# Optimization experiments

Hardware: AMD Instinct MI355X
Metric: run time of the kernel (lower is better)

Reference implementation:

```python
import jax, jax.numpy as jnp
import numpy as np

T, B, NA = 32, 32, 5          # timesteps, envs, actions
HID, FEAT = 256, 512          # lstm hidden, cnn features
IN_DIM = FEAT + NA            # lstm input size (517)
FLAT = 64 * 7 * 7             # cnn flatten size (3136)


def _conv(x, w, b, s):
    # x: NCHW, w: OIHW, VALID padding, stride s
    y = jax.lax.conv_general_dilated(x, w, (s, s), 'VALID',
                                     dimension_numbers=('NCHW', 'OIHW', 'NCHW'))
    return y + b[None, :, None, None]


def setup_inputs() -> dict:
    key = jax.random.key(0)
    ks = jax.random.split(key, 24)
    p = lambda k, shape: (jax.random.normal(k, shape, jnp.float32) * 0.05)
    return {
        'image': jax.random.uniform(ks[0], (T * B, 3, 84, 84), jnp.float32) * 255.0,
        'last_action': jax.random.randint(ks[1], (T * B,), 0, NA),
        'done': jax.random.bernoulli(ks[2], 0.05, (T * B,)).astype(jnp.float32),
        'h0': jnp.zeros((B, HID), jnp.float32),
        'c0': jnp.zeros((B, HID), jnp.float32),
        # NatureCNN params
        'W1': p(ks[3], (32, 3, 8, 8)), 'b1': jnp.zeros((32,), jnp.float32),
        'W2': p(ks[4], (64, 32, 4, 4)), 'b2': jnp.zeros((64,), jnp.float32),
        'W3': p(ks[5], (64, 64, 3, 3)), 'b3': jnp.zeros((64,), jnp.float32),
        'Wfc': p(ks[6], (FEAT, FLAT)), 'bfc': jnp.zeros((FEAT,), jnp.float32),
        # LSTM params (torch gate order i,f,g,o)
        'W_ih': p(ks[7], (4 * HID, IN_DIM)), 'W_hh': p(ks[8], (4 * HID, HID)),
        'b_ih': jnp.zeros((4 * HID,), jnp.float32), 'b_hh': jnp.zeros((4 * HID,), jnp.float32),
        # policy MLP (hidden 64, tanh)
        'Wp1': p(ks[9], (64, HID)), 'bp1': jnp.zeros((64,), jnp.float32),
        'Wp2': p(ks[10], (NA, 64)) * 0.01, 'bp2': jnp.zeros((NA,), jnp.float32),
        # value MLP
        'Wv1': p(ks[11], (64, HID)), 'bv1': jnp.zeros((64,), jnp.float32),
        'Wv2': p(ks[12], (1, 64)), 'bv2': jnp.zeros((1,), jnp.float32),
    }


def reference(image, last_action, done, h0, c0,
              W1, b1, W2, b2, W3, b3, Wfc, bfc,
              W_ih, W_hh, b_ih, b_hh,
              Wp1, bp1, Wp2, bp2, Wv1, bv1, Wv2, bv2):
    # --- extract: NatureCNN + one-hot(last_action) ---
    x = image / 255.0
    x = jax.nn.relu(_conv(x, W1, b1, 4))   # (TB,32,20,20)
    x = jax.nn.relu(_conv(x, W2, b2, 2))   # (TB,64,9,9)
    x = jax.nn.relu(_conv(x, W3, b3, 1))   # (TB,64,7,7)
    x = x.reshape(x.shape[0], -1)
    feat = jax.nn.relu(x @ Wfc.T + bfc)    # (TB,512)
    oh = jax.nn.one_hot(last_action, NA, dtype=feat.dtype)
    xs = jnp.concatenate([feat, oh], axis=1).reshape(T, B, IN_DIM)
    ds = done.reshape(T, B)

    # --- remember: done-masked LSTM recurrence (torch gate order i,f,g,o) ---
    def step(carry, inp):
        h, c = carry
        xt, dt = inp
        m = (1.0 - dt)[:, None]
        h = h * m
        c = c * m
        g = xt @ W_ih.T + b_ih + h @ W_hh.T + b_hh   # (B, 4*HID)
        i, f, gg, o = jnp.split(g, 4, axis=1)
        c = jax.nn.sigmoid(f) * c + jax.nn.sigmoid(i) * jnp.tanh(gg)
        h = jax.nn.sigmoid(o) * jnp.tanh(c)
        return (h, c), h

    (hT, cT), hs = jax.lax.scan(step, (h0, c0), (xs, ds))
    h = hs.reshape(T * B, HID)

    # --- heads ---
    logits = jnp.tanh(h @ Wp1.T + bp1) @ Wp2.T + bp2   # (TB, NA)
    v = jnp.tanh(h @ Wv1.T + bv1) @ Wv2.T + bv2        # (TB, 1)
    return logits, v, hT, cT
```

## Files before the change

### kernel.cpp

```cpp
#include <hip/hip_runtime.h>
#include <math.h>

typedef float  f4v __attribute__((ext_vector_type(4)));
typedef short  s8v __attribute__((ext_vector_type(8)));
typedef int    i4v __attribute__((ext_vector_type(4)));

__device__ __forceinline__ float sigm(float x) { return 1.f / (1.f + expf(-x)); }
__device__ __forceinline__ unsigned short f2bf(float f) {
    unsigned int u = __float_as_uint(f);
    return (unsigned short)((u + 0x7FFF + ((u >> 16) & 1)) >> 16);
}
__device__ __forceinline__ unsigned int cvt2(float lo, float hi) {
    unsigned int r;
    asm("v_cvt_pk_bf16_f32 %0, %1, %2" : "=v"(r) : "v"(lo), "v"(hi));
    return r;
}
__device__ __forceinline__ s8v pack8(float4 a, float4 b) {
    union { unsigned int u[4]; s8v v; } r;
    r.u[0] = cvt2(a.x, a.y); r.u[1] = cvt2(a.z, a.w);
    r.u[2] = cvt2(b.x, b.y); r.u[3] = cvt2(b.z, b.w);
    return r.v;
}

__global__ __launch_bounds__(256) void k_amax(const float* __restrict__ Whh,
                                              unsigned int* __restrict__ amax_bits) {
    int i = blockIdx.x * 256 + threadIdx.x;
    float v = fabsf(Whh[i]);
#pragma unroll
    for (int o = 1; o < 64; o <<= 1) v = fmaxf(v, __shfl_xor(v, o));
    if ((threadIdx.x & 63) == 0) atomicMax(amax_bits, __float_as_uint(v));
}

__global__ __launch_bounds__(256) void k_prep(const float* __restrict__ W2, const float* __restrict__ W3,
                                              const float* __restrict__ Wfc, const float* __restrict__ Wih,
                                              const float* __restrict__ W1, const float* __restrict__ Whh,
                                              const unsigned int* __restrict__ amax_bits,
                                              unsigned short* __restrict__ W2p, unsigned short* __restrict__ W3p,
                                              unsigned short* __restrict__ Wfcp, unsigned short* __restrict__ Wihp,
                                              unsigned short* __restrict__ W1p, signed char* __restrict__ Wq) {
    int i = blockIdx.x * 256 + threadIdx.x;
    if (i < 32768) {
        W2p[i] = f2bf(W2[i]);
    } else if (i < 98304) {
        int j = i - 32768;
        int co = j >> 10, r = j & 1023, ci = r >> 4, s = r & 15, ky = s >> 2, kx = s & 3;
        W3p[j] = (ky < 3 && kx < 3) ? f2bf(W3[((co * 64 + ci) * 3 + ky) * 3 + kx]) : (unsigned short)0;
    } else if (i < 1703936) {
        int j = i - 98304;
        Wfcp[j] = f2bf(Wfc[j]);
    } else if (i < 2228224) {
        int j = i - 1703936;
        int n = j >> 9, k = j & 511;
        Wihp[j] = f2bf(Wih[n * 517 + k]);
    } else if (i < 2234368) {
        int j = i - 2228224;
        W1p[j] = f2bf(W1[j] * (1.f / 255.f));
    } else if (i < 2496512) {
        int j = i - 2234368;
        float amax = __uint_as_float(amax_bits[0]);
        float s = 127.f / amax;
        int qv = (int)rintf(Whh[j] * s);
        qv = qv > 127 ? 127 : (qv < -127 ? -127 : qv);
        Wq[j] = (signed char)qv;
    }
}

__global__ __launch_bounds__(256) void k_conv1(const float* __restrict__ img,
                                               const unsigned short* __restrict__ Bw,
                                               const float* __restrict__ bias,
                                               unsigned short* __restrict__ out) {
    __shared__ unsigned short c1s[32][132];
    int lane = threadIdx.x & 63, w = threadIdx.x >> 6;
    int l15 = lane & 15, q = lane >> 4;
    int m0 = blockIdx.x * 128;
    const float* Ap[2];
#pragma unroll
    for (int mf = 0; mf < 2; ++mf) {
        int m = m0 + w * 32 + mf * 16 + l15;
        int im = m / 400, p = m - im * 400;
        int oy = p / 20, ox = p - oy * 20;
        Ap[mf] = img + im * 21168 + oy * 336 + ox * 4;
    }
    const unsigned short* Bp0 = Bw + l15 * 192 + q * 8;
    const unsigned short* Bp1 = Bw + (16 + l15) * 192 + q * 8;
    s8v bf0[6], bf1[6];
#pragma unroll
    for (int ks = 0; ks < 6; ++ks) {
        bf0[ks] = *(const s8v*)(Bp0 + ks * 32);
        bf1[ks] = *(const s8v*)(Bp1 + ks * 32);
    }
    int roffs[6];
#pragma unroll
    for (int ks = 0; ks < 6; ++ks) {
        int k0 = ks * 32 + q * 8;
        int c = k0 >> 6, ky = (k0 >> 3) & 7;
        roffs[ks] = c * 7056 + ky * 84;
    }
    f4v acc[4];
#pragma unroll
    for (int i = 0; i < 4; ++i) acc[i] = (f4v){0.f, 0.f, 0.f, 0.f};
    float4 ca[2], cb[2];
#pragma unroll
    for (int mf = 0; mf < 2; ++mf) {
        ca[mf] = *(const float4*)(Ap[mf] + roffs[0]);
        cb[mf] = *(const float4*)(Ap[mf] + roffs[0] + 4);
    }
#pragma unroll
    for (int ks = 0; ks < 6; ++ks) {
        float4 na[2], nb[2];
        if (ks < 5) {
#pragma unroll
            for (int mf = 0; mf < 2; ++mf) {
                na[mf] = *(const float4*)(Ap[mf] + roffs[ks + 1]);
                nb[mf] = *(const float4*)(Ap[mf] + roffs[ks + 1] + 4);
            }
        }
#pragma unroll
        for (int mf = 0; mf < 2; ++mf) {
            s8v ua = pack8(ca[mf], cb[mf]);
            acc[mf * 2 + 0] = __builtin_amdgcn_mfma_f32_16x16x32_bf16(ua, bf0[ks], acc[mf * 2 + 0], 0, 0, 0);
            acc[mf * 2 + 1] = __builtin_amdgcn_mfma_f32_16x16x32_bf16(ua, bf1[ks], acc[mf * 2 + 1], 0, 0, 0);
        }
        if (ks < 5) {
#pragma unroll
            for (int mf = 0; mf < 2; ++mf) { ca[mf] = na[mf]; cb[mf] = nb[mf]; }
        }
    }
#pragma unroll
    for (int nf = 0; nf < 2; ++nf) {
        int n = nf * 16 + l15;
        float b = bias[n];
#pragma unroll
        for (int mf = 0; mf < 2; ++mf) {
            int ml = w * 32 + mf * 16 + q * 4;
#pragma unroll
            for (int r = 0; r < 4; r += 2) {
                float v0 = acc[mf * 2 + nf][r] + b;     v0 = v0 > 0.f ? v0 : 0.f;
                float v1 = acc[mf * 2 + nf][r + 1] + b; v1 = v1 > 0.f ? v1 : 0.f;
                *(unsigned int*)&c1s[n][ml + r] = cvt2(v0, v1);
            }
        }
    }
    __syncthreads();
#pragma unroll
    for (int seg = 0; seg < 16; ++seg) {
        int flat = seg * 256 + threadIdx.x;
        int n = flat >> 7, ml = flat & 127;
        int m = m0 + ml;
        int im = m / 400, p = m - im * 400;
        out[(im * 32 + n) * 400 + p] = c1s[n][ml];
    }
}

__global__ __launch_bounds__(256) void k_conv2(const unsigned short* __restrict__ A,
                                               const unsigned short* __restrict__ Bw,
                                               const float* __restrict__ bias,
                                               unsigned short* __restrict__ out) {
    __shared__ unsigned short c2s[32][136];
    int lane = threadIdx.x & 63, w = threadIdx.x >> 6;
    int l15 = lane & 15, q = lane >> 4;
    int m0 = blockIdx.x * 128;
    int n0 = blockIdx.y * 32;
    int ma = m0 + w * 32 + l15, mb = ma + 16;
    int ia = ma / 81, pa = ma - ia * 81; int oya = pa / 9, oxa = pa - oya * 9;
    int ib = mb / 81, pb = mb - ib * 81; int oyb = pb / 9, oxb = pb - oyb * 9;
    const unsigned short* Aa = A + ia * 12800 + oya * 40 + oxa * 2 + (q & 1) * 40;
    const unsigned short* Ab = A + ib * 12800 + oyb * 40 + oxb * 2 + (q & 1) * 40;
    int ci0 = q >> 1;
    const unsigned short* B0 = Bw + (n0 + l15) * 512 + q * 8;
    const unsigned short* B1 = B0 + 16 * 512;
    f4v acc[4];
#pragma unroll
    for (int i = 0; i < 4; ++i) acc[i] = (f4v){0.f, 0.f, 0.f, 0.f};
    union AU { unsigned int u[4]; s8v v; };
    const unsigned short* pa_ = Aa + ci0 * 400;
    const unsigned short* pb_ = Ab + ci0 * 400;
    AU ua, ub;
    ua.u[0] = *(const unsigned int*)(pa_);      ua.u[1] = *(const unsigned int*)(pa_ + 2);
    ua.u[2] = *(const unsigned int*)(pa_ + 20); ua.u[3] = *(const unsigned int*)(pa_ + 22);
    ub.u[0] = *(const unsigned int*)(pb_);      ub.u[1] = *(const unsigned int*)(pb_ + 2);
    ub.u[2] = *(const unsigned int*)(pb_ + 20); ub.u[3] = *(const unsigned int*)(pb_ + 22);
    s8v b0 = *(const s8v*)B0, b1 = *(const s8v*)B1;
    for (int c = 0; c < 16; ++c) {
        AU nua, nub; s8v nb0, nb1;
        if (c < 15) {
            pa_ += 800; pb_ += 800; B0 += 32; B1 += 32;
            nua.u[0] = *(const unsigned int*)(pa_);      nua.u[1] = *(const unsigned int*)(pa_ + 2);
            nua.u[2] = *(const unsigned int*)(pa_ + 20); nua.u[3] = *(const unsigned int*)(pa_ + 22);
            nub.u[0] = *(const unsigned int*)(pb_);      nub.u[1] = *(const unsigned int*)(pb_ + 2);
            nub.u[2] = *(const unsigned int*)(pb_ + 20); nub.u[3] = *(const unsigned int*)(pb_ + 22);
            nb0 = *(const s8v*)B0; nb1 = *(const s8v*)B1;
        }
        acc[0] = __builtin_amdgcn_mfma_f32_16x16x32_bf16(ua.v, b0, acc[0], 0, 0, 0);
        acc[1] = __builtin_amdgcn_mfma_f32_16x16x32_bf16(ua.v, b1, acc[1], 0, 0, 0);
        acc[2] = __builtin_amdgcn_mfma_f32_16x16x32_bf16(ub.v, b0, acc[2], 0, 0, 0);
        acc[3] = __builtin_amdgcn_mfma_f32_16x16x32_bf16(ub.v, b1, acc[3], 0, 0, 0);
        if (c < 15) { ua = nua; ub = nub; b0 = nb0; b1 = nb1; }
    }
#pragma unroll
    for (int nf = 0; nf < 2; ++nf) {
        int nl = nf * 16 + l15;
        float b = bias[n0 + nl];
#pragma unroll
        for (int mf = 0; mf < 2; ++mf) {
            int ml = w * 32 + mf * 16 + q * 4;
#pragma unroll
            for (int r = 0; r < 4; r += 2) {
                float v0 = acc[mf * 2 + nf][r] + b;     v0 = v0 > 0.f ? v0 : 0.f;
                float v1 = acc[mf * 2 + nf][r + 1] + b; v1 = v1 > 0.f ? v1 : 0.f;
                *(unsigned int*)&c2s[nl][ml + r] = cvt2(v0, v1);
            }
        }
    }
    __syncthreads();
#pragma unroll
    for (int seg = 0; seg < 16; ++seg) {
        int flat = seg * 256 + threadIdx.x;
        int nl = flat >> 7, ml = flat & 127;
        int n = n0 + nl;
        int m = m0 + ml;
        int im = m / 81, p = m - im * 81;
        out[im * 5184 + n * 81 + p] = c2s[nl][ml];
    }
}

__global__ __launch_bounds__(256) void k_conv3(const unsigned short* __restrict__ A,
                                               const unsigned short* __restrict__ Bw,
                                               const float* __restrict__ bias,
                                               unsigned short* __restrict__ out) {
    __shared__ unsigned short c3s[32][68];
    int lane = threadIdx.x & 63, w = threadIdx.x >> 6;
    int l15 = lane & 15, q = lane >> 4;
    int m0 = blockIdx.x * 64;
    int n0 = blockIdx.y * 32;
    int ma = m0 + w * 16 + l15;
    int ia = ma / 49, pa = ma - ia * 49; int oya = pa / 7, oxa = pa - oya * 7;
    int ky0 = (q & 1) * 2;
    int r0off = ky0 * 9;
    int r1off = (ky0 + 1 > 2 ? 2 : ky0 + 1) * 9;
    int zr = q & 1;
    const unsigned short* Aa = A + ia * 5184 + oya * 9 + oxa;
    int ci0 = q >> 1;
    const unsigned short* B0 = Bw + (n0 + l15) * 1024 + q * 8;
    const unsigned short* B1 = B0 + 16 * 1024;
    f4v acc[2];
    acc[0] = (f4v){0.f, 0.f, 0.f, 0.f};
    acc[1] = (f4v){0.f, 0.f, 0.f, 0.f};
    const unsigned short* pa_ = Aa + ci0 * 81;
    unsigned short ca_[6];
    ca_[0] = pa_[r0off]; ca_[1] = pa_[r0off + 1]; ca_[2] = pa_[r0off + 2];
    ca_[3] = pa_[r1off]; ca_[4] = pa_[r1off + 1]; ca_[5] = pa_[r1off + 2];
    s8v b0 = *(const s8v*)B0, b1 = *(const s8v*)B1;
    for (int c = 0; c < 32; ++c) {
        unsigned short na_[6]; s8v nb0, nb1;
        if (c < 31) {
            pa_ += 162; B0 += 32; B1 += 32;
            na_[0] = pa_[r0off]; na_[1] = pa_[r0off + 1]; na_[2] = pa_[r0off + 2];
            na_[3] = pa_[r1off]; na_[4] = pa_[r1off + 1]; na_[5] = pa_[r1off + 2];
            nb0 = *(const s8v*)B0; nb1 = *(const s8v*)B1;
        }
        s8v av;
        av[0] = (short)ca_[0]; av[1] = (short)ca_[1]; av[2] = (short)ca_[2]; av[3] = 0;
        av[4] = zr ? (short)0 : (short)ca_[3];
        av[5] = zr ? (short)0 : (short)ca_[4];
        av[6] = zr ? (short)0 : (short)ca_[5];
        av[7] = 0;
        acc[0] = __builtin_amdgcn_mfma_f32_16x16x32_bf16(av, b0, acc[0], 0, 0, 0);
        acc[1] = __builtin_amdgcn_mfma_f32_16x16x32_bf16(av, b1, acc[1], 0, 0, 0);
        if (c < 31) {
#pragma unroll
            for (int j = 0; j < 6; ++j) ca_[j] = na_[j];
            b0 = nb0; b1 = nb1;
        }
    }
#pragma unroll
    for (int nf = 0; nf < 2; ++nf) {
        int nl = nf * 16 + l15;
        float b = bias[n0 + nl];
        int ml = w * 16 + q * 4;
#pragma unroll
        for (int r = 0; r < 4; r += 2) {
            float v0 = acc[nf][r] + b;     v0 = v0 > 0.f ? v0 : 0.f;
            float v1 = acc[nf][r + 1] + b; v1 = v1 > 0.f ? v1 : 0.f;
            *(unsigned int*)&c3s[nl][ml + r] = cvt2(v0, v1);
        }
    }
    __syncthreads();
#pragma unroll
    for (int seg = 0; seg < 8; ++seg) {
        int flat = seg * 256 + threadIdx.x;
        int nl = flat >> 6, ml = flat & 63;
        int n = n0 + nl;
        int m = m0 + ml;
        int im = m / 49, p = m - im * 49;
        out[im * 3136 + n * 49 + p] = c3s[nl][ml];
    }
}

__global__ __launch_bounds__(256) void k_fc(const unsigned short* __restrict__ A,
                                            const unsigned short* __restrict__ Bw,
                                            const float* __restrict__ bias,
                                            unsigned short* __restrict__ out) {
    int lane = threadIdx.x & 63, w = threadIdx.x >> 6;
    int l15 = lane & 15, q = lane >> 4;
    int m0 = blockIdx.x * 32 + (w & 1) * 16;
    int n0 = blockIdx.y * 64 + (w >> 1) * 32;
    const unsigned short* Ap = A + (m0 + l15) * 3136 + q * 8;
    const unsigned short* B0 = Bw + (n0 + l15) * 3136 + q * 8;
    const unsigned short* B1 = B0 + 16 * 3136;
    f4v acc0 = (f4v){0.f, 0.f, 0.f, 0.f}, acc1 = (f4v){0.f, 0.f, 0.f, 0.f};
    s8v av = *(const s8v*)Ap, b0 = *(const s8v*)B0, b1 = *(const s8v*)B1;
    for (int c = 0; c < 97; ++c) {
        Ap += 32; B0 += 32; B1 += 32;
        s8v nav = *(const s8v*)Ap, nb0 = *(const s8v*)B0, nb1 = *(const s8v*)B1;
        acc0 = __builtin_amdgcn_mfma_f32_16x16x32_bf16(av, b0, acc0, 0, 0, 0);
        acc1 = __builtin_amdgcn_mfma_f32_16x16x32_bf16(av, b1, acc1, 0, 0, 0);
        av = nav; b0 = nb0; b1 = nb1;
    }
    acc0 = __builtin_amdgcn_mfma_f32_16x16x32_bf16(av, b0, acc0, 0, 0, 0);
    acc1 = __builtin_amdgcn_mfma_f32_16x16x32_bf16(av, b1, acc1, 0, 0, 0);
    float bi0 = bias[n0 + l15], bi1 = bias[n0 + 16 + l15];
#pragma unroll
    for (int r = 0; r < 4; ++r) {
        int m = m0 + q * 4 + r;
        float v0 = acc0[r] + bi0; v0 = v0 > 0.f ? v0 : 0.f;
        float v1 = acc1[r] + bi1; v1 = v1 > 0.f ? v1 : 0.f;
        out[m * 512 + n0 + l15] = f2bf(v0);
        out[m * 512 + n0 + 16 + l15] = f2bf(v1);
    }
}

__global__ __launch_bounds__(256) void k_gx(const unsigned short* __restrict__ A,
                                            const unsigned short* __restrict__ Bw,
                                            const float* __restrict__ Wih,
                                            const float* __restrict__ bih,
                                            const float* __restrict__ bhh,
                                            const int* __restrict__ act,
                                            float* __restrict__ out) {
    int lane = threadIdx.x & 63, w = threadIdx.x >> 6;
    int l15 = lane & 15, q = lane >> 4;
    int m0 = blockIdx.x * 32 + (w & 1) * 16;
    int n0 = blockIdx.y * 64 + (w >> 1) * 32;
    const unsigned short* Ap = A + (m0 + l15) * 512 + q * 8;
    const unsigned short* B0 = Bw + (n0 + l15) * 512 + q * 8;
    const unsigned short* B1 = B0 + 16 * 512;
    f4v acc0 = (f4v){0.f, 0.f, 0.f, 0.f}, acc1 = (f4v){0.f, 0.f, 0.f, 0.f};
    for (int c = 0; c < 16; ++c) {
        s8v av = *(const s8v*)Ap;
        s8v b0 = *(const s8v*)B0;
        s8v b1 = *(const s8v*)B1;
        Ap += 32; B0 += 32; B1 += 32;
        acc0 = __builtin_amdgcn_mfma_f32_16x16x32_bf16(av, b0, acc0, 0, 0, 0);
        acc1 = __builtin_amdgcn_mfma_f32_16x16x32_bf16(av, b1, acc1, 0, 0, 0);
    }
    int na = n0 + l15, nb = n0 + 16 + l15;
    float ca = bih[na] + bhh[na], cb_ = bih[nb] + bhh[nb];
#pragma unroll
    for (int r = 0; r < 4; ++r) {
        int m = m0 + q * 4 + r;
        int a = act[m];
        out[m * 1024 + na] = acc0[r] + Wih[na * 517 + 512 + a] + ca;
        out[m * 1024 + nb] = acc1[r] + Wih[nb * 517 + 512 + a] + cb_;
    }
}

__global__ __launch_bounds__(1024) void k_lstm_all(const float* __restrict__ h0,
                                                   const float* __restrict__ c0,
                                                   const float* __restrict__ done,
                                                   const float* __restrict__ gx,
                                                   const signed char* __restrict__ Wq,
                                                   const unsigned int* __restrict__ amax_bits,
                                                   float* __restrict__ hs,
                                                   float* __restrict__ cb) {
    int b = blockIdx.x;
    int tid = threadIdx.x;
    int w = tid >> 6, lane = tid & 63;
    int l15 = lane & 15, q = lane >> 4;
    __shared__ float gbuf[1024];
    __shared__ float cst[256];
    __shared__ signed char hA[4][64][16];

    i4v wfr[4][4];
    const signed char* wb = Wq + (w * 64 + l15) * 256 + q * 16;
#pragma unroll
    for (int s = 0; s < 4; ++s)
#pragma unroll
        for (int kf = 0; kf < 4; ++kf)
            wfr[s][kf] = *(const i4v*)(wb + s * 16 * 256 + kf * 64);
    float sw = __uint_as_float(amax_bits[0]) * (1.f / (127.f * 127.f));

    ((int*)hA)[tid] = 0;
    __syncthreads();
    if (tid < 256) {
        int u = tid;
        cst[u] = c0[b * 256 + u];
        float m0v = 1.f - done[b];
        float hv = h0[b * 256 + u] * m0v;
        hv = hv > 1.f ? 1.f : (hv < -1.f ? -1.f : hv);
        hA[u >> 6][((u >> 4) & 3) * 16][u & 15] = (signed char)(int)rintf(hv * 127.f);
    }
    __syncthreads();

    for (int t = 0; t < 32; ++t) {
        float gxi = 0.f, gxf = 0.f, gxg = 0.f, gxo = 0.f, dcur = 0.f, dnxt = 0.f;
        if (tid < 256) {
            const float* gr = gx + (t * 32 + b) * 1024;
            gxi = gr[tid]; gxf = gr[256 + tid]; gxg = gr[512 + tid]; gxo = gr[768 + tid];
            dcur = done[t * 32 + b];
            dnxt = (t < 31) ? done[(t + 1) * 32 + b] : 1.f;
        }
        i4v acc[4];
#pragma unroll
        for (int s = 0; s < 4; ++s) acc[s] = (i4v){0, 0, 0, 0};
#pragma unroll
        for (int kf = 0; kf < 4; ++kf) {
            i4v a = *(const i4v*)&hA[kf][lane][0];
#pragma unroll
            for (int s = 0; s < 4; ++s)
                acc[s] = __builtin_amdgcn_mfma_i32_16x16x64_i8(a, wfr[s][kf], acc[s], 0, 0, 0);
        }
        if (q == 0) {
#pragma unroll
            for (int s = 0; s < 4; ++s)
                gbuf[w * 64 + s * 16 + l15] = (float)acc[s][0];
        }
        __syncthreads();
        if (tid < 256) {
            int u = tid;
            float gi = gbuf[u] * sw + gxi;
            float gf = gbuf[256 + u] * sw + gxf;
            float gg = gbuf[512 + u] * sw + gxg;
            float go = gbuf[768 + u] * sw + gxo;
            float cm = cst[u] * (1.f - dcur);
            float cn = sigm(gf) * cm + sigm(gi) * tanhf(gg);
            float hn = sigm(go) * tanhf(cn);
            cst[u] = cn;
            hs[t * 8192 + b * 256 + u] = hn;
            float hv = hn * (1.f - dnxt);
            hA[u >> 6][((u >> 4) & 3) * 16][u & 15] = (signed char)(int)rintf(hv * 127.f);
        }
        __syncthreads();
    }
    if (tid < 256) cb[b * 256 + tid] = cst[tid];
}

__global__ __launch_bounds__(256) void k_heads(const float* __restrict__ hs,
                                               const float* __restrict__ cb,
                                               const float* __restrict__ Wp1, const float* __restrict__ bp1,
                                               const float* __restrict__ Wp2, const float* __restrict__ bp2,
                                               const float* __restrict__ Wv1, const float* __restrict__ bv1,
                                               const float* __restrict__ Wv2, const float* __restrict__ bv2,
                                               float* __restrict__ out) {
    int lane = threadIdx.x & 63;
    int m = blockIdx.x * 4 + (threadIdx.x >> 6);
    const float4* hv = (const float4*)(hs + m * 256);
    const float4* wp = (const float4*)(Wp1 + lane * 256);
    const float4* wq = (const float4*)(Wv1 + lane * 256);
    float ap = 0.f, av = 0.f;
#pragma unroll 8
    for (int k = 0; k < 64; ++k) {
        float4 h4 = hv[k];
        float4 p4 = wp[k];
        float4 q4 = wq[k];
        ap += h4.x * p4.x + h4.y * p4.y + h4.z * p4.z + h4.w * p4.w;
        av += h4.x * q4.x + h4.y * q4.y + h4.z * q4.z + h4.w * q4.w;
    }
    float hp = tanhf(ap + bp1[lane]);
    float hq = tanhf(av + bv1[lane]);
#pragma unroll
    for (int j = 0; j < 5; ++j) {
        float s = hp * Wp2[j * 64 + lane];
        s += __shfl_xor(s, 1); s += __shfl_xor(s, 2); s += __shfl_xor(s, 4);
        s += __shfl_xor(s, 8); s += __shfl_xor(s, 16); s += __shfl_xor(s, 32);
        if (lane == 0) out[m * 5 + j] = s + bp2[j];
    }
    float s = hq * Wv2[lane];
    s += __shfl_xor(s, 1); s += __shfl_xor(s, 2); s += __shfl_xor(s, 4);
    s += __shfl_xor(s, 8); s += __shfl_xor(s, 16); s += __shfl_xor(s, 32);
    if (lane == 0) out[5120 + m] = s + bv2[0];

    int g = blockIdx.x * 256 + threadIdx.x;
    if (g < 8192) {
        out[6144 + g] = hs[31 * 8192 + g];
        out[6144 + 8192 + g] = cb[g];
    }
}

extern "C" void kernel_launch(void* const* d_in, const int* in_sizes, int n_in,
                              void* d_out, int out_size, void* d_ws, size_t ws_size,
                              hipStream_t stream) {
    const float* image = (const float*)d_in[0];
    const int*   act   = (const int*)d_in[1];
    const float* done  = (const float*)d_in[2];
    const float* h0    = (const float*)d_in[3];
    const float* c0    = (const float*)d_in[4];
    const float* W1    = (const float*)d_in[5];
    const float* b1    = (const float*)d_in[6];
    const float* W2    = (const float*)d_in[7];
    const float* b2    = (const float*)d_in[8];
    const float* W3    = (const float*)d_in[9];
    const float* b3    = (const float*)d_in[10];
    const float* Wfc   = (const float*)d_in[11];
    const float* bfc   = (const float*)d_in[12];
    const float* Wih   = (const float*)d_in[13];
    const float* Whh   = (const float*)d_in[14];
    const float* bih   = (const float*)d_in[15];
    const float* bhh   = (const float*)d_in[16];
    const float* Wp1   = (const float*)d_in[17];
    const float* bp1   = (const float*)d_in[18];
    const float* Wp2   = (const float*)d_in[19];
    const float* bp2   = (const float*)d_in[20];
    const float* Wv1   = (const float*)d_in[21];
    const float* bv1   = (const float*)d_in[22];
    const float* Wv2   = (const float*)d_in[23];
    const float* bv2   = (const float*)d_in[24];
    float* out = (float*)d_out;
    char* base = (char*)d_ws;

    unsigned short* a1   = (unsigned short*)(base);
    unsigned short* a2   = (unsigned short*)(base + 26214432);
    unsigned short* W2p  = (unsigned short*)(base + 36831328);
    unsigned short* W3p  = W2p + 32768;
    unsigned short* Wfcp = W2p + 98304;
    unsigned short* Wihp = W2p + 1703936;
    unsigned short* W1p  = (unsigned short*)(base + 41287776);
    unsigned int*   amax = (unsigned int*)(base + 41300064);
    signed char*    Wq   = (signed char*)(base + 41300096);
    unsigned short* a3   = (unsigned short*)(base);
    unsigned short* feat = (unsigned short*)(base + 6422528);
    float* gx = (float*)(base + 7471104);
    float* hs = (float*)(base + 11665408);
    float* cb = (float*)(base + 12713984);

    hipMemsetAsync(amax, 0, 4, stream);
    k_amax<<<1024, 256, 0, stream>>>(Whh, amax);
    k_prep<<<9752, 256, 0, stream>>>(W2, W3, Wfc, Wih, W1, Whh, amax, W2p, W3p, Wfcp, Wihp, W1p, Wq);
    k_conv1<<<3200, 256, 0, stream>>>(image, W1p, b1, a1);
    k_conv2<<<dim3(648, 2), 256, 0, stream>>>(a1, W2p, b2, a2);
    k_conv3<<<dim3(784, 2), 256, 0, stream>>>(a2, W3p, b3, a3);
    k_fc<<<dim3(32, 8), 256, 0, stream>>>(a3, Wfcp, bfc, feat);
    k_gx<<<dim3(32, 16), 256, 0, stream>>>(feat, Wihp, Wih, bih, bhh, act, gx);
    k_lstm_all<<<32, 1024, 0, stream>>>(h0, c0, done, gx, Wq, amax, hs, cb);
    k_heads<<<256, 256, 0, stream>>>(hs, cb, Wp1, bp1, Wp2, bp2, Wv1, bv1, Wv2, bv2, out);
}
```

Baseline: 485.6 us.

## Stage conv2/conv3 input images in swizzled LDS and compute all channels per block

conv2 and conv3 now load two whole images' activations into LDS with an XOR swizzle and a channel-innermost layout. Each block then computes all 64 output channels with implicit-GEMM MFMAs over kernel taps, instead of gathering scattered 2-byte global loads per K-chunk across two channel-half blocks. Weights are repacked in prep into tap-major, channel-inner order, and conv3's zero padding of its 3x3 taps to 16 is removed. conv1's explicit software prefetch is dropped in favour of direct loads. The risks are higher LDS use per block, limiting occupancy, and redundant MFMA work on padded rows in partial tiles.

```diff
diff --git a/kernel.cpp b/kernel.cpp
--- a/kernel.cpp
+++ b/kernel.cpp
@@ -40,23 +40,25 @@
                                               unsigned short* __restrict__ W1p, signed char* __restrict__ Wq) {
     int i = blockIdx.x * 256 + threadIdx.x;
     if (i < 32768) {
-        W2p[i] = f2bf(W2[i]);
-    } else if (i < 98304) {
+        int co = i >> 9, k = i & 511, t = k >> 5, ci = k & 31, ky = t >> 2, kx = t & 3;
+        W2p[i] = f2bf(W2[co * 512 + ci * 16 + ky * 4 + kx]);
+    } else if (i < 69632) {
         int j = i - 32768;
-        int co = j >> 10, r = j & 1023, ci = r >> 4, s = r & 15, ky = s >> 2, kx = s & 3;
-        W3p[j] = (ky < 3 && kx < 3) ? f2bf(W3[((co * 64 + ci) * 3 + ky) * 3 + kx]) : (unsigned short)0;
-    } else if (i < 1703936) {
-        int j = i - 98304;
+        int co = j / 576, k = j - co * 576, t = k >> 6, ci = k & 63;
+        int ky = t / 3, kx = t - ky * 3;
+        W3p[j] = f2bf(W3[((co * 64 + ci) * 3 + ky) * 3 + kx]);
+    } else if (i < 1675264) {
+        int j = i - 69632;
         Wfcp[j] = f2bf(Wfc[j]);
-    } else if (i < 2228224) {
-        int j = i - 1703936;
+    } else if (i < 2199552) {
+        int j = i - 1675264;
         int n = j >> 9, k = j & 511;
         Wihp[j] = f2bf(Wih[n * 517 + k]);
-    } else if (i < 2234368) {
-        int j = i - 2228224;
+    } else if (i < 2205696) {
+        int j = i - 2199552;
         W1p[j] = f2bf(W1[j] * (1.f / 255.f));
-    } else if (i < 2496512) {
-        int j = i - 2234368;
+    } else if (i < 2467840) {
+        int j = i - 2205696;
         float amax = __uint_as_float(amax_bits[0]);
         float s = 127.f / amax;
         int qv = (int)rintf(Whh[j] * s);
@@ -99,31 +101,15 @@
     f4v acc[4];
 #pragma unroll
     for (int i = 0; i < 4; ++i) acc[i] = (f4v){0.f, 0.f, 0.f, 0.f};
-    float4 ca[2], cb[2];
-#pragma unroll
-    for (int mf = 0; mf < 2; ++mf) {
-        ca[mf] = *(const float4*)(Ap[mf] + roffs[0]);
-        cb[mf] = *(const float4*)(Ap[mf] + roffs[0] + 4);
-    }
 #pragma unroll
     for (int ks = 0; ks < 6; ++ks) {
-        float4 na[2], nb[2];
-        if (ks < 5) {
-#pragma unroll
-            for (int mf = 0; mf < 2; ++mf) {
-                na[mf] = *(const float4*)(Ap[mf] + roffs[ks + 1]);
-                nb[mf] = *(const float4*)(Ap[mf] + roffs[ks + 1] + 4);
-            }
-        }
 #pragma unroll
         for (int mf = 0; mf < 2; ++mf) {
-            s8v ua = pack8(ca[mf], cb[mf]);
+            float4 a0 = *(const float4*)(Ap[mf] + roffs[ks]);
+            float4 a1 = *(const float4*)(Ap[mf] + roffs[ks] + 4);
+            s8v ua = pack8(a0, a1);
             acc[mf * 2 + 0] = __builtin_amdgcn_mfma_f32_16x16x32_bf16(ua, bf0[ks], acc[mf * 2 + 0], 0, 0, 0);
             acc[mf * 2 + 1] = __builtin_amdgcn_mfma_f32_16x16x32_bf16(ua, bf1[ks], acc[mf * 2 + 1], 0, 0, 0);
-        }
-        if (ks < 5) {
-#pragma unroll
-            for (int mf = 0; mf < 2; ++mf) { ca[mf] = na[mf]; cb[mf] = nb[mf]; }
         }
     }
 #pragma unroll
@@ -152,148 +138,188 @@
     }
 }
 
-__global__ __launch_bounds__(256) void k_conv2(const unsigned short* __restrict__ A,
-                                               const unsigned short* __restrict__ Bw,
-                                               const float* __restrict__ bias,
-                                               unsigned short* __restrict__ out) {
-    __shared__ unsigned short c2s[32][136];
-    int lane = threadIdx.x & 63, w = threadIdx.x >> 6;
+__global__ __launch_bounds__(256, 2) void k_conv2(const unsigned short* __restrict__ A,
+                                                  const unsigned short* __restrict__ Bw,
+                                                  const float* __restrict__ bias,
+                                                  unsigned short* __restrict__ out) {
+    __shared__ unsigned short sA[800 * 32];
+    __shared__ unsigned short c2s[64][196];
+    int tid = threadIdx.x;
+    int lane = tid & 63, w = tid >> 6;
     int l15 = lane & 15, q = lane >> 4;
-    int m0 = blockIdx.x * 128;
-    int n0 = blockIdx.y * 32;
-    int ma = m0 + w * 32 + l15, mb = ma + 16;
-    int ia = ma / 81, pa = ma - ia * 81; int oya = pa / 9, oxa = pa - oya * 9;
-    int ib = mb / 81, pb = mb - ib * 81; int oyb = pb / 9, oxb = pb - oyb * 9;
-    const unsigned short* Aa = A + ia * 12800 + oya * 40 + oxa * 2 + (q & 1) * 40;
-    const unsigned short* Ab = A + ib * 12800 + oyb * 40 + oxb * 2 + (q & 1) * 40;
-    int ci0 = q >> 1;
-    const unsigned short* B0 = Bw + (n0 + l15) * 512 + q * 8;
-    const unsigned short* B1 = B0 + 16 * 512;
-    f4v acc[4];
-#pragma unroll
-    for (int i = 0; i < 4; ++i) acc[i] = (f4v){0.f, 0.f, 0.f, 0.f};
-    union AU { unsigned int u[4]; s8v v; };
-    const unsigned short* pa_ = Aa + ci0 * 400;
-    const unsigned short* pb_ = Ab + ci0 * 400;
-    AU ua, ub;
-    ua.u[0] = *(const unsigned int*)(pa_);      ua.u[1] = *(const unsigned int*)(pa_ + 2);
-    ua.u[2] = *(const unsigned int*)(pa_ + 20); ua.u[3] = *(const unsigned int*)(pa_ + 22);
-    ub.u[0] = *(const unsigned int*)(pb_);      ub.u[1] = *(const unsigned int*)(pb_ + 2);
-    ub.u[2] = *(const unsigned int*)(pb_ + 20); ub.u[3] = *(const unsigned int*)(pb_ + 22);
-    s8v b0 = *(const s8v*)B0, b1 = *(const s8v*)B1;
-    for (int c = 0; c < 16; ++c) {
-        AU nua, nub; s8v nb0, nb1;
-        if (c < 15) {
-            pa_ += 800; pb_ += 800; B0 += 32; B1 += 32;
-            nua.u[0] = *(const unsigned int*)(pa_);      nua.u[1] = *(const unsigned int*)(pa_ + 2);
-            nua.u[2] = *(const unsigned int*)(pa_ + 20); nua.u[3] = *(const unsigned int*)(pa_ + 22);
-            nub.u[0] = *(const unsigned int*)(pb_);      nub.u[1] = *(const unsigned int*)(pb_ + 2);
-            nub.u[2] = *(const unsigned int*)(pb_ + 20); nub.u[3] = *(const unsigned int*)(pb_ + 22);
-            nb0 = *(const s8v*)B0; nb1 = *(const s8v*)B1;
-        }
-        acc[0] = __builtin_amdgcn_mfma_f32_16x16x32_bf16(ua.v, b0, acc[0], 0, 0, 0);
-        acc[1] = __builtin_amdgcn_mfma_f32_16x16x32_bf16(ua.v, b1, acc[1], 0, 0, 0);
-        acc[2] = __builtin_amdgcn_mfma_f32_16x16x32_bf16(ub.v, b0, acc[2], 0, 0, 0);
-        acc[3] = __builtin_amdgcn_mfma_f32_16x16x32_bf16(ub.v, b1, acc[3], 0, 0, 0);
-        if (c < 15) { ua = nua; ub = nub; b0 = nb0; b1 = nb1; }
-    }
-#pragma unroll
-    for (int nf = 0; nf < 2; ++nf) {
-        int nl = nf * 16 + l15;
-        float b = bias[n0 + nl];
+    int img0 = blockIdx.x * 2;
+    char* sAb = (char*)sA;
+    const s8v* srcv = (const s8v*)(A + img0 * 12800);
+    for (int wi = tid; wi < 3200; wi += 256) {
+        s8v v = srcv[wi];
+        int f = wi * 8;
+        int im = f / 12800, r = f - im * 12800, ci = r / 400, p = r - ci * 400;
+#pragma unroll
+        for (int j = 0; j < 8; ++j) {
+            int R = im * 400 + p + j;
+            int Rl = (R >> 1) + (R & 1) * 400;
+            int by = (Rl * 32 + ci) * 2 ^ ((Rl & 7) << 4);
+            *(unsigned short*)(sAb + by) = (unsigned short)v[j];
+        }
+    }
+    __syncthreads();
+    int Rb[3];
+#pragma unroll
+    for (int mf = 0; mf < 3; ++mf) {
+        int t = w * 3 + mf;
+        int im = t / 6;
+        int pp = (t - im * 6) * 16 + l15;
+        int px = pp > 80 ? 80 : pp;
+        int oy = px / 9, ox = px - oy * 9;
+        Rb[mf] = im * 400 + oy * 40 + ox * 2;
+    }
+    const unsigned short* Bp0 = Bw + l15 * 512 + q * 8;
+    const unsigned short* Bp1 = Bw + (16 + l15) * 512 + q * 8;
+    const unsigned short* Bp2 = Bw + (32 + l15) * 512 + q * 8;
+    const unsigned short* Bp3 = Bw + (48 + l15) * 512 + q * 8;
+    f4v acc[3][4];
+#pragma unroll
+    for (int i = 0; i < 3; ++i)
+#pragma unroll
+        for (int j = 0; j < 4; ++j) acc[i][j] = (f4v){0.f, 0.f, 0.f, 0.f};
+#pragma unroll
+    for (int s = 0; s < 16; ++s) {
+        const int ky = s >> 2, kx = s & 3;
+        const int d = ky * 20 + kx;
+        s8v a[3];
+#pragma unroll
+        for (int mf = 0; mf < 3; ++mf) {
+            int R = Rb[mf] + d;
+            int Rl = (R >> 1) + (R & 1) * 400;
+            int by = (Rl * 64 + q * 16) ^ ((Rl & 7) << 4);
+            a[mf] = *(const s8v*)(sAb + by);
+        }
+        s8v b0 = *(const s8v*)(Bp0 + s * 32);
+        s8v b1 = *(const s8v*)(Bp1 + s * 32);
+        s8v b2 = *(const s8v*)(Bp2 + s * 32);
+        s8v b3 = *(const s8v*)(Bp3 + s * 32);
+#pragma unroll
+        for (int mf = 0; mf < 3; ++mf) {
+            acc[mf][0] = __builtin_amdgcn_mfma_f32_16x16x32_bf16(a[mf], b0, acc[mf][0], 0, 0, 0);
+            acc[mf][1] = __builtin_amdgcn_mfma_f32_16x16x32_bf16(a[mf], b1, acc[mf][1], 0, 0, 0);
+            acc[mf][2] = __builtin_amdgcn_mfma_f32_16x16x32_bf16(a[mf], b2, acc[mf][2], 0, 0, 0);
+            acc[mf][3] = __builtin_amdgcn_mfma_f32_16x16x32_bf16(a[mf], b3, acc[mf][3], 0, 0, 0);
+        }
+    }
+#pragma unroll
+    for (int nf = 0; nf < 4; ++nf) {
+        int co = nf * 16 + l15;
+        float b = bias[co];
+#pragma unroll
+        for (int mf = 0; mf < 3; ++mf) {
+            int rr = (w * 3 + mf) * 16 + q * 4;
+#pragma unroll
+            for (int r = 0; r < 4; r += 2) {
+                float v0 = acc[mf][nf][r] + b;     v0 = v0 > 0.f ? v0 : 0.f;
+                float v1 = acc[mf][nf][r + 1] + b; v1 = v1 > 0.f ? v1 : 0.f;
+                *(unsigned int*)&c2s[co][rr + r] = cvt2(v0, v1);
+            }
+        }
+    }
+    __syncthreads();
+    for (int idx = tid; idx < 10368; idx += 256) {
+        int im = idx / 5184, r2 = idx - im * 5184, co = r2 / 81, p = r2 - co * 81;
+        out[(img0 + im) * 5184 + r2] = c2s[co][im * 96 + p];
+    }
+}
+
+__global__ __launch_bounds__(256, 2) void k_conv3(const unsigned short* __restrict__ A,
+                                                  const unsigned short* __restrict__ Bw,
+                                                  const float* __restrict__ bias,
+                                                  unsigned short* __restrict__ out) {
+    __shared__ unsigned short sA[162 * 64];
+    __shared__ unsigned short c3s[64][132];
+    int tid = threadIdx.x;
+    int lane = tid & 63, w = tid >> 6;
+    int l15 = lane & 15, q = lane >> 4;
+    int img0 = blockIdx.x * 2;
+    char* sAb = (char*)sA;
+    const s8v* srcv = (const s8v*)(A + img0 * 5184);
+    for (int wi = tid; wi < 1296; wi += 256) {
+        s8v v = srcv[wi];
+        int f = wi * 8;
+#pragma unroll
+        for (int j = 0; j < 8; ++j) {
+            int fe = f + j;
+            int im = fe / 5184, r = fe - im * 5184, ci = r / 81, p = r - ci * 81;
+            int R = im * 81 + p;
+            int by = (R * 64 + ci) * 2 ^ ((R & 7) << 4);
+            *(unsigned short*)(sAb + by) = (unsigned short)v[j];
+        }
+    }
+    __syncthreads();
+    int Rb[2];
+#pragma unroll
+    for (int mf = 0; mf < 2; ++mf) {
+        int t = w * 2 + mf;
+        int im = t >> 2;
+        int pp = (t & 3) * 16 + l15;
+        int px = pp > 48 ? 48 : pp;
+        int oy = px / 7, ox = px - oy * 7;
+        Rb[mf] = im * 81 + oy * 9 + ox;
+    }
+    const unsigned short* Bp0 = Bw + l15 * 576 + q * 8;
+    const unsigned short* Bp1 = Bw + (16 + l15) * 576 + q * 8;
+    const unsigned short* Bp2 = Bw + (32 + l15) * 576 + q * 8;
+    const unsigned short* Bp3 = Bw + (48 + l15) * 576 + q * 8;
+    f4v acc[2][4];
+#pragma unroll
+    for (int i = 0; i < 2; ++i)
+#pragma unroll
+        for (int j = 0; j < 4; ++j) acc[i][j] = (f4v){0.f, 0.f, 0.f, 0.f};
+#pragma unroll
+    for (int s = 0; s < 18; ++s) {
+        const int tap = s >> 1, cb2 = (s & 1) * 64;
+        const int ky = tap / 3, kx = tap - ky * 3;
+        const int d = ky * 9 + kx;
+        s8v a0, a1;
+        {
+            int R = Rb[0] + d;
+            int by = (R * 128 + cb2 + q * 16) ^ ((R & 7) << 4);
+            a0 = *(const s8v*)(sAb + by);
+        }
+        {
+            int R = Rb[1] + d;
+            int by = (R * 128 + cb2 + q * 16) ^ ((R & 7) << 4);
+            a1 = *(const s8v*)(sAb + by);
+        }
+        s8v b0 = *(const s8v*)(Bp0 + s * 32);
+        s8v b1 = *(const s8v*)(Bp1 + s * 32);
+        s8v b2 = *(const s8v*)(Bp2 + s * 32);
+        s8v b3 = *(const s8v*)(Bp3 + s * 32);
+        acc[0][0] = __builtin_amdgcn_mfma_f32_16x16x32_bf16(a0, b0, acc[0][0], 0, 0, 0);
+        acc[0][1] = __builtin_amdgcn_mfma_f32_16x16x32_bf16(a0, b1, acc[0][1], 0, 0, 0);
+        acc[0][2] = __builtin_amdgcn_mfma_f32_16x16x32_bf16(a0, b2, acc[0][2], 0, 0, 0);
+        acc[0][3] = __builtin_amdgcn_mfma_f32_16x16x32_bf16(a0, b3, acc[0][3], 0, 0, 0);
+        acc[1][0] = __builtin_amdgcn_mfma_f32_16x16x32_bf16(a1, b0, acc[1][0], 0, 0, 0);
+        acc[1][1] = __builtin_amdgcn_mfma_f32_16x16x32_bf16(a1, b1, acc[1][1], 0, 0, 0);
+        acc[1][2] = __builtin_amdgcn_mfma_f32_16x16x32_bf16(a1, b2, acc[1][2], 0, 0, 0);
+        acc[1][3] = __builtin_amdgcn_mfma_f32_16x16x32_bf16(a1, b3, acc[1][3], 0, 0, 0);
+    }
+#pragma unroll
+    for (int nf = 0; nf < 4; ++nf) {
+        int co = nf * 16 + l15;
+        float b = bias[co];
 #pragma unroll
         for (int mf = 0; mf < 2; ++mf) {
-            int ml = w * 32 + mf * 16 + q * 4;
+            int rr = (w * 2 + mf) * 16 + q * 4;
 #pragma unroll
             for (int r = 0; r < 4; r += 2) {
-                float v0 = acc[mf * 2 + nf][r] + b;     v0 = v0 > 0.f ? v0 : 0.f;
-                float v1 = acc[mf * 2 + nf][r + 1] + b; v1 = v1 > 0.f ? v1 : 0.f;
-                *(unsigned int*)&c2s[nl][ml + r] = cvt2(v0, v1);
+                float v0 = acc[mf][nf][r] + b;     v0 = v0 > 0.f ? v0 : 0.f;
+                float v1 = acc[mf][nf][r + 1] + b; v1 = v1 > 0.f ? v1 : 0.f;
+                *(unsigned int*)&c3s[co][rr + r] = cvt2(v0, v1);
             }
         }
     }
     __syncthreads();
-#pragma unroll
-    for (int seg = 0; seg < 16; ++seg) {
-        int flat = seg * 256 + threadIdx.x;
-        int nl = flat >> 7, ml = flat & 127;
-        int n = n0 + nl;
-        int m = m0 + ml;
-        int im = m / 81, p = m - im * 81;
-        out[im * 5184 + n * 81 + p] = c2s[nl][ml];
-    }
-}
-
-__global__ __launch_bounds__(256) void k_conv3(const unsigned short* __restrict__ A,
-                                               const unsigned short* __restrict__ Bw,
-                                               const float* __restrict__ bias,
-                                               unsigned short* __restrict__ out) {
-    __shared__ unsigned short c3s[32][68];
-    int lane = threadIdx.x & 63, w = threadIdx.x >> 6;
-    int l15 = lane & 15, q = lane >> 4;
-    int m0 = blockIdx.x * 64;
-    int n0 = blockIdx.y * 32;
-    int ma = m0 + w * 16 + l15;
-    int ia = ma / 49, pa = ma - ia * 49; int oya = pa / 7, oxa = pa - oya * 7;
-    int ky0 = (q & 1) * 2;
-    int r0off = ky0 * 9;
-    int r1off = (ky0 + 1 > 2 ? 2 : ky0 + 1) * 9;
-    int zr = q & 1;
-    const unsigned short* Aa = A + ia * 5184 + oya * 9 + oxa;
-    int ci0 = q >> 1;
-    const unsigned short* B0 = Bw + (n0 + l15) * 1024 + q * 8;
-    const unsigned short* B1 = B0 + 16 * 1024;
-    f4v acc[2];
-    acc[0] = (f4v){0.f, 0.f, 0.f, 0.f};
-    acc[1] = (f4v){0.f, 0.f, 0.f, 0.f};
-    const unsigned short* pa_ = Aa + ci0 * 81;
-    unsigned short ca_[6];
-    ca_[0] = pa_[r0off]; ca_[1] = pa_[r0off + 1]; ca_[2] = pa_[r0off + 2];
-    ca_[3] = pa_[r1off]; ca_[4] = pa_[r1off + 1]; ca_[5] = pa_[r1off + 2];
-    s8v b0 = *(const s8v*)B0, b1 = *(const s8v*)B1;
-    for (int c = 0; c < 32; ++c) {
-        unsigned short na_[6]; s8v nb0, nb1;
-        if (c < 31) {
-            pa_ += 162; B0 += 32; B1 += 32;
-            na_[0] = pa_[r0off]; na_[1] = pa_[r0off + 1]; na_[2] = pa_[r0off + 2];
-            na_[3] = pa_[r1off]; na_[4] = pa_[r1off + 1]; na_[5] = pa_[r1off + 2];
-            nb0 = *(const s8v*)B0; nb1 = *(const s8v*)B1;
-        }
-        s8v av;
-        av[0] = (short)ca_[0]; av[1] = (short)ca_[1]; av[2] = (short)ca_[2]; av[3] = 0;
-        av[4] = zr ? (short)0 : (short)ca_[3];
-        av[5] = zr ? (short)0 : (short)ca_[4];
-        av[6] = zr ? (short)0 : (short)ca_[5];
-        av[7] = 0;
-        acc[0] = __builtin_amdgcn_mfma_f32_16x16x32_bf16(av, b0, acc[0], 0, 0, 0);
-        acc[1] = __builtin_amdgcn_mfma_f32_16x16x32_bf16(av, b1, acc[1], 0, 0, 0);
-        if (c < 31) {
-#pragma unroll
-            for (int j = 0; j < 6; ++j) ca_[j] = na_[j];
-            b0 = nb0; b1 = nb1;
-        }
-    }
-#pragma unroll
-    for (int nf = 0; nf < 2; ++nf) {
-        int nl = nf * 16 + l15;
-        float b = bias[n0 + nl];
-        int ml = w * 16 + q * 4;
-#pragma unroll
-        for (int r = 0; r < 4; r += 2) {
-            float v0 = acc[nf][r] + b;     v0 = v0 > 0.f ? v0 : 0.f;
-            float v1 = acc[nf][r + 1] + b; v1 = v1 > 0.f ? v1 : 0.f;
-            *(unsigned int*)&c3s[nl][ml + r] = cvt2(v0, v1);
-        }
-    }
-    __syncthreads();
-#pragma unroll
-    for (int seg = 0; seg < 8; ++seg) {
-        int flat = seg * 256 + threadIdx.x;
-        int nl = flat >> 6, ml = flat & 63;
-        int n = n0 + nl;
-        int m = m0 + ml;
-        int im = m / 49, p = m - im * 49;
-        out[im * 3136 + n * 49 + p] = c3s[nl][ml];
+    for (int idx = tid; idx < 6272; idx += 256) {
+        int im = idx / 3136, r2 = idx - im * 3136, co = r2 / 49, p = r2 - co * 49;
+        out[(img0 + im) * 3136 + r2] = c3s[co][im * 64 + p];
     }
 }
 
@@ -520,12 +546,12 @@
     unsigned short* a1   = (unsigned short*)(base);
     unsigned short* a2   = (unsigned short*)(base + 26214432);
     unsigned short* W2p  = (unsigned short*)(base + 36831328);
-    unsigned short* W3p  = W2p + 32768;
-    unsigned short* Wfcp = W2p + 98304;
-    unsigned short* Wihp = W2p + 1703936;
-    unsigned short* W1p  = (unsigned short*)(base + 41287776);
-    unsigned int*   amax = (unsigned int*)(base + 41300064);
-    signed char*    Wq   = (signed char*)(base + 41300096);
+    unsigned short* W3p  = (unsigned short*)(base + 36896864);
+    unsigned short* Wfcp = (unsigned short*)(base + 36970592);
+    unsigned short* Wihp = (unsigned short*)(base + 40181856);
+    unsigned short* W1p  = (unsigned short*)(base + 41230432);
+    unsigned int*   amax = (unsigned int*)(base + 41242752);
+    signed char*    Wq   = (signed char*)(base + 41242784);
     unsigned short* a3   = (unsigned short*)(base);
     unsigned short* feat = (unsigned short*)(base + 6422528);
     float* gx = (float*)(base + 7471104);
@@ -534,10 +560,10 @@
 
     hipMemsetAsync(amax, 0, 4, stream);
     k_amax<<<1024, 256, 0, stream>>>(Whh, amax);
-    k_prep<<<9752, 256, 0, stream>>>(W2, W3, Wfc, Wih, W1, Whh, amax, W2p, W3p, Wfcp, Wihp, W1p, Wq);
+    k_prep<<<9640, 256, 0, stream>>>(W2, W3, Wfc, Wih, W1, Whh, amax, W2p, W3p, Wfcp, Wihp, W1p, Wq);
     k_conv1<<<3200, 256, 0, stream>>>(image, W1p, b1, a1);
-    k_conv2<<<dim3(648, 2), 256, 0, stream>>>(a1, W2p, b2, a2);
-    k_conv3<<<dim3(784, 2), 256, 0, stream>>>(a2, W3p, b3, a3);
+    k_conv2<<<512, 256, 0, stream>>>(a1, W2p, b2, a2);
+    k_conv3<<<512, 256, 0, stream>>>(a2, W3p, b3, a3);
     k_fc<<<dim3(32, 8), 256, 0, stream>>>(a3, Wfcp, bfc, feat);
     k_gx<<<dim3(32, 16), 256, 0, stream>>>(feat, Wihp, Wih, bih, bhh, act, gx);
     k_lstm_all<<<32, 1024, 0, stream>>>(h0, c0, done, gx, Wq, amax, hs, cb);
```

New measurement: 431.9 us. 11.1% less time.
